# Optimization experiments

Hardware: AMD Instinct MI355X
Metric: run time of the kernel (lower is better)

The kernel has to match this reference:

```python
import jax, jax.numpy as jnp
import numpy as np
from jax import lax

KERNEL = 5
PAD = 2
STRIDE = 1


def setup_inputs() -> dict:
    key = jax.random.key(0)
    kx, kw = jax.random.split(key)
    x = jax.random.uniform(kx, (8, 1, 480, 640), dtype=jnp.float32)  # depth map in [0,1)
    # kaiming_normal_ on (1, 64, 5, 5): fan_in = 64*5*5 per torch's convention for this layout
    fan_in = 64 * KERNEL * KERNEL
    std = np.sqrt(2.0 / fan_in)
    weight = jax.random.normal(kw, (1, 64, KERNEL, KERNEL), dtype=jnp.float32) * std
    return {"x": x, "weight": weight}


def reference(x, weight):
    B, C, H, W = x.shape
    k, p, s = KERNEL, PAD, STRIDE
    # im2col, channel ordering (C, kh, kw) matches torch.nn.functional.unfold
    patches = lax.conv_general_dilated_patches(
        x, (k, k), (s, s), ((p, p), (p, p))
    )  # [B, C*k*k, Ho, Wo]
    Ho, Wo = patches.shape[2], patches.shape[3]
    x_uf = patches.reshape(B, C * k * k, Ho * Wo)  # [B, K, L]
    zero_mask = (x_uf > 1e-4).astype(x.dtype)
    x_ref = jnp.sum(x_uf, axis=1, keepdims=True) / (
        jnp.sum(zero_mask, axis=1, keepdims=True) + 1e-6
    )  # per-patch mean over valid pixels
    x_norm = (x_ref - x_uf) * zero_mask  # [B, K, L]
    w = weight.reshape(weight.shape[1], -1)  # [O, K] (same flat layout as torch view)
    out = jnp.einsum("ok,bkl->bol", w, x_norm)  # [B, O, L]
    return out.reshape(B, -1, H // s, W // s)
```

## Files before the change

### kernel.cpp

```cpp
#include <hip/hip_runtime.h>

#define IH 480
#define IW 640
#define NB 8
#define OC 64
#define KK 5
#define PD 2

__global__ __launch_bounds__(256) void ndconv_kernel(
    const float* __restrict__ x,
    const float* __restrict__ wgt,
    float* __restrict__ out)
{
    int idx = blockIdx.x * blockDim.x + threadIdx.x;
    if (idx >= NB * IH * IW) return;
    int w = idx % IW;
    int t = idx / IW;
    int h = t % IH;
    int b = t / IH;

    const float* xb = x + (size_t)b * (IH * IW);

    float patch[KK * KK];
    float sum = 0.0f;
    float cnt = 0.0f;
#pragma unroll
    for (int kh = 0; kh < KK; ++kh) {
        int hh = h + kh - PD;
        bool hv = (unsigned)hh < (unsigned)IH;
#pragma unroll
        for (int kw = 0; kw < KK; ++kw) {
            int ww = w + kw - PD;
            bool v = hv && ((unsigned)ww < (unsigned)IW);
            float val = v ? xb[hh * IW + ww] : 0.0f;
            patch[kh * KK + kw] = val;
            sum += val;
            cnt += (val > 1e-4f) ? 1.0f : 0.0f;
        }
    }
    float mean = sum / (cnt + 1e-6f);

#pragma unroll
    for (int k = 0; k < KK * KK; ++k) {
        float v = patch[k];
        patch[k] = (v > 1e-4f) ? (mean - v) : 0.0f;
    }

    float* ob = out + (size_t)b * OC * (IH * IW) + (size_t)h * IW + w;

#pragma unroll 4
    for (int o = 0; o < OC; ++o) {
        const float* wo = wgt + o * (KK * KK);
        float acc = 0.0f;
#pragma unroll
        for (int k = 0; k < KK * KK; ++k)
            acc = fmaf(wo[k], patch[k], acc);
        ob[(size_t)o * (IH * IW)] = acc;
    }
}

extern "C" void kernel_launch(void* const* d_in, const int* in_sizes, int n_in,
                              void* d_out, int out_size, void* d_ws, size_t ws_size,
                              hipStream_t stream) {
    const float* x   = (const float*)d_in[0];
    const float* wgt = (const float*)d_in[1];
    float* out = (float*)d_out;

    const int total = NB * IH * IW;
    const int block = 256;
    const int grid = (total + block - 1) / block;
    ndconv_kernel<<<grid, block, 0, stream>>>(x, wgt, out);
}
```

Baseline: 655.0 us.

## Compute four adjacent pixels per thread with vectorized nontemporal stores

Each thread now handles four consecutive output pixels, loading a shared 5x8 input window once and reusing each weight load across four FMAs. Outputs go out as 128-bit nontemporal vector stores, which cuts store instruction count and keeps the large output stream from polluting cache. In exchange register pressure rises (100 patch values plus the input window) and there are four times fewer threads, which may reduce occupancy.

```diff
diff --git a/kernel.cpp b/kernel.cpp
--- a/kernel.cpp
+++ b/kernel.cpp
@@ -6,56 +6,95 @@
 #define OC 64
 #define KK 5
 #define PD 2
+#define PX 4
+#define WT (IW / PX)
+
+typedef float vfloat4 __attribute__((ext_vector_type(4)));
 
 __global__ __launch_bounds__(256) void ndconv_kernel(
     const float* __restrict__ x,
     const float* __restrict__ wgt,
     float* __restrict__ out)
 {
-    int idx = blockIdx.x * blockDim.x + threadIdx.x;
-    if (idx >= NB * IH * IW) return;
-    int w = idx % IW;
-    int t = idx / IW;
-    int h = t % IH;
-    int b = t / IH;
+    int t = blockIdx.x * blockDim.x + threadIdx.x;
+    if (t >= NB * IH * WT) return;
+    int wt = t % WT;
+    int r  = t / WT;
+    int h  = r % IH;
+    int b  = r / IH;
+    int w0 = wt * PX;
 
     const float* xb = x + (size_t)b * (IH * IW);
 
-    float patch[KK * KK];
-    float sum = 0.0f;
-    float cnt = 0.0f;
+    int   ccol[PX + KK - 1];
+    bool  cok [PX + KK - 1];
+#pragma unroll
+    for (int j = 0; j < PX + KK - 1; ++j) {
+        int c = w0 - PD + j;
+        cok[j]  = (unsigned)c < (unsigned)IW;
+        ccol[j] = min(max(c, 0), IW - 1);
+    }
+
+    float v[KK][PX + KK - 1];
 #pragma unroll
     for (int kh = 0; kh < KK; ++kh) {
-        int hh = h + kh - PD;
+        int hh  = h + kh - PD;
         bool hv = (unsigned)hh < (unsigned)IH;
+        const float* xr = xb + min(max(hh, 0), IH - 1) * IW;
+#pragma unroll
+        for (int j = 0; j < PX + KK - 1; ++j) {
+            float val = xr[ccol[j]];
+            v[kh][j]  = (hv && cok[j]) ? val : 0.0f;
+        }
+    }
+
+    float sum[PX] = {0.f, 0.f, 0.f, 0.f};
+    float cnt[PX] = {0.f, 0.f, 0.f, 0.f};
+#pragma unroll
+    for (int kh = 0; kh < KK; ++kh)
+#pragma unroll
+        for (int kw = 0; kw < KK; ++kw)
+#pragma unroll
+            for (int px = 0; px < PX; ++px) {
+                float val = v[kh][kw + px];
+                sum[px] += val;
+                cnt[px] += (val > 1e-4f) ? 1.0f : 0.0f;
+            }
+
+    float mean[PX];
+#pragma unroll
+    for (int px = 0; px < PX; ++px)
+        mean[px] = sum[px] / (cnt[px] + 1e-6f);
+
+    vfloat4 q[KK * KK];
+#pragma unroll
+    for (int kh = 0; kh < KK; ++kh)
 #pragma unroll
         for (int kw = 0; kw < KK; ++kw) {
-            int ww = w + kw - PD;
-            bool v = hv && ((unsigned)ww < (unsigned)IW);
-            float val = v ? xb[hh * IW + ww] : 0.0f;
-            patch[kh * KK + kw] = val;
-            sum += val;
-            cnt += (val > 1e-4f) ? 1.0f : 0.0f;
+            int k = kh * KK + kw;
+#pragma unroll
+            for (int px = 0; px < PX; ++px) {
+                float val = v[kh][kw + px];
+                q[k][px] = (val > 1e-4f) ? (mean[px] - val) : 0.0f;
+            }
         }
-    }
-    float mean = sum / (cnt + 1e-6f);
 
-#pragma unroll
-    for (int k = 0; k < KK * KK; ++k) {
-        float v = patch[k];
-        patch[k] = (v > 1e-4f) ? (mean - v) : 0.0f;
-    }
+    float* ob = out + (size_t)b * OC * (IH * IW) + (size_t)h * IW + w0;
 
-    float* ob = out + (size_t)b * OC * (IH * IW) + (size_t)h * IW + w;
-
-#pragma unroll 4
+#pragma unroll 2
     for (int o = 0; o < OC; ++o) {
         const float* wo = wgt + o * (KK * KK);
-        float acc = 0.0f;
+        vfloat4 acc = (vfloat4)0.0f;
 #pragma unroll
-        for (int k = 0; k < KK * KK; ++k)
-            acc = fmaf(wo[k], patch[k], acc);
-        ob[(size_t)o * (IH * IW)] = acc;
+        for (int k = 0; k < KK * KK; ++k) {
+            float wk = wo[k];
+            acc[0] = fmaf(wk, q[k][0], acc[0]);
+            acc[1] = fmaf(wk, q[k][1], acc[1]);
+            acc[2] = fmaf(wk, q[k][2], acc[2]);
+            acc[3] = fmaf(wk, q[k][3], acc[3]);
+        }
+        __builtin_nontemporal_store(
+            acc, reinterpret_cast<vfloat4*>(ob + (size_t)o * (IH * IW)));
     }
 }
 
@@ -66,8 +105,8 @@
     const float* wgt = (const float*)d_in[1];
     float* out = (float*)d_out;
 
-    const int total = NB * IH * IW;
+    const int total = NB * IH * WT;
     const int block = 256;
-    const int grid = (total + block - 1) / block;
+    const int grid  = (total + block - 1) / block;
     ndconv_kernel<<<grid, block, 0, stream>>>(x, wgt, out);
 }
```

Result: faster. 636.6 us (-2.8%).
